# Optimization experiments

Measured on AMD Instinct MI355X. Metric: run time of the kernel, lower is better.

The kernel has to match this reference:

```python
import jax, jax.numpy as jnp
import numpy as np

S, HID, H, KV, D = 2048, 3584, 16, 8, 256
WINDOW = 1024
SOFTCAP = 50.0
SCALING = 256 ** (-0.5)  # query_pre_attn_scalar ** -0.5
EPS = 1e-6
ROPE_THETA = 10000.0


def _rope_tables(seq_len, dim, theta):
    inv_freq = 1.0 / (theta ** (np.arange(0, dim, 2, dtype=np.float32) / dim))
    t = np.arange(seq_len, dtype=np.float32)
    freqs = np.outer(t, inv_freq)            # [S, D/2]
    emb = np.concatenate([freqs, freqs], -1)  # [S, D]
    return jnp.asarray(np.cos(emb)), jnp.asarray(np.sin(emb))


def setup_inputs() -> dict:
    key = jax.random.key(0)
    ks = jax.random.split(key, 3)
    hidden_states = jax.random.normal(ks[0], (S, HID), jnp.float32)
    w_qkv = jax.random.normal(ks[1], (HID, (H + 2 * KV) * D), jnp.float32) * (HID ** -0.5)
    w_o = jax.random.normal(ks[2], (H * D, HID), jnp.float32) * ((H * D) ** -0.5)
    q_norm_w = jnp.zeros((D,), jnp.float32)  # gemma norm stores weight as (1 + w)
    k_norm_w = jnp.zeros((D,), jnp.float32)
    cos, sin = _rope_tables(S, D, ROPE_THETA)
    return {"hidden_states": hidden_states, "w_qkv": w_qkv, "w_o": w_o,
            "q_norm_w": q_norm_w, "k_norm_w": k_norm_w, "cos": cos, "sin": sin}


def _rms_norm(x, w):
    # gemma-style: fp32 norm, scale by (1 + w); x: [S, h, D]
    xf = x.astype(jnp.float32)
    var = jnp.mean(xf * xf, axis=-1, keepdims=True)
    return (xf * jax.lax.rsqrt(var + EPS) * (1.0 + w)).astype(x.dtype)


def _rotate_half(x):
    x1, x2 = jnp.split(x, 2, axis=-1)
    return jnp.concatenate([-x2, x1], axis=-1)


def _apply_rope(x, cos, sin):
    # x: [S, h, D]; cos/sin: [S, D]
    c = cos[:, None, :]
    s = sin[:, None, :]
    return x * c + _rotate_half(x) * s


def reference(hidden_states, w_qkv, w_o, q_norm_w, k_norm_w, cos, sin):
    qkv = hidden_states @ w_qkv                      # [S, (H+2KV)*D]
    q = qkv[:, : H * D].reshape(S, H, D)
    k = qkv[:, H * D: (H + KV) * D].reshape(S, KV, D)
    v = qkv[:, (H + KV) * D:].reshape(S, KV, D)

    q = _rms_norm(q, q_norm_w)                       # gemma3 q_norm
    k = _rms_norm(k, k_norm_w)                       # gemma3 k_norm
    q = _apply_rope(q, cos, sin)
    k = _apply_rope(k, cos, sin)

    # GQA: expand KV heads to H
    rep = H // KV
    k = jnp.repeat(k, rep, axis=1)                   # [S, H, D]
    v = jnp.repeat(v, rep, axis=1)

    scores = jnp.einsum('shd,thd->hst', q, k) * SCALING  # [H, S, S]
    scores = SOFTCAP * jnp.tanh(scores / SOFTCAP)        # logit softcapping

    i = jnp.arange(S)[:, None]
    j = jnp.arange(S)[None, :]
    allowed = (j <= i) & ((i - j) < WINDOW)              # causal + sliding window
    scores = jnp.where(allowed[None], scores, jnp.float32(-1e30))

    attn = jax.nn.softmax(scores, axis=-1)
    out = jnp.einsum('hst,thd->shd', attn, v).reshape(S, H * D)
    return out @ w_o                                     # [S, HID]
```

## Files before the change

### kernel.cpp

```cpp
#include <hip/hip_runtime.h>
#include <hip/hip_bf16.h>
#include <math.h>

typedef __attribute__((ext_vector_type(8))) short short8;
typedef __attribute__((ext_vector_type(4))) float floatx4;
typedef unsigned short u16;

typedef __attribute__((address_space(1))) const void* gas_ptr;
typedef __attribute__((address_space(3))) void* las_ptr;

__device__ __forceinline__ float bf2f(u16 h) {
  union { unsigned u; float f; } v; v.u = ((unsigned)h) << 16; return v.f;
}
__device__ __forceinline__ u16 f2bf(float f) {
  union { float f; unsigned u; } v; v.f = f;
  unsigned r = v.u + 0x7FFFu + ((v.u >> 16) & 1u);
  return (u16)(r >> 16);
}
__device__ __forceinline__ float ldf_dyn(const void* p, size_t i, bool f32) {
  return f32 ? ((const float*)p)[i] : bf2f(((const u16*)p)[i]);
}
__device__ __forceinline__ short8 load8_dyn(const void* p, size_t idx, bool f32) {
  if (f32) {
    const float* f = (const float*)p;
    float4 a = *(const float4*)(f + idx);
    float4 b = *(const float4*)(f + idx + 4);
    short8 r;
    r[0] = (short)f2bf(a.x); r[1] = (short)f2bf(a.y);
    r[2] = (short)f2bf(a.z); r[3] = (short)f2bf(a.w);
    r[4] = (short)f2bf(b.x); r[5] = (short)f2bf(b.y);
    r[6] = (short)f2bf(b.z); r[7] = (short)f2bf(b.w);
    return r;
  }
  return *(const short8*)((const u16*)p + idx);
}
__device__ __forceinline__ void gl_lds16(const u16* g, u16* l) {
  __builtin_amdgcn_global_load_lds((gas_ptr)g, (las_ptr)l, 16, 0, 0);
}

__global__ void probe_dtype_kernel(const void* hidden, int* flag) {
  __shared__ int cnt;
  if (threadIdx.x == 0) cnt = 0;
  __syncthreads();
  const u16* h = (const u16*)hidden;
  int local = 0;
  for (int i = threadIdx.x; i < 8192; i += 256) {
    u16 u = h[i];
    int e = (u >> 7) & 0xFF;
    if ((e >= 64 && e <= 160) || (u & 0x7FFF) == 0) local++;
  }
  atomicAdd(&cnt, local);
  __syncthreads();
  if (threadIdx.x == 0) *flag = (cnt < 7700) ? 1 : 0;
}

__global__ __launch_bounds__(256) void convert_dyn_kernel(
    const void* __restrict__ src, u16* __restrict__ dst, size_t n,
    const int* __restrict__ flagp)
{
  if (*flagp == 0) return;
  size_t i = ((size_t)blockIdx.x * 256 + threadIdx.x) * 8;
  if (i < n) *(short8*)(dst + i) = load8_dyn(src, i, true);
}

__global__ __launch_bounds__(256) void transpose_dyn_kernel(
    const void* __restrict__ src, u16* __restrict__ dst, int R, int C,
    const int* __restrict__ flagp)
{
  const bool f32 = (*flagp != 0);
  const int c0 = blockIdx.x * 64, r0 = blockIdx.y * 64;
  __shared__ __attribute__((aligned(16))) u16 T[64][72];
  const int tid = threadIdx.x;
#pragma unroll
  for (int i = 0; i < 2; i++) {
    int t = tid + i * 256;
    int r = t >> 3, cc = (t & 7) << 3;
    *(short8*)(&T[r][cc]) = load8_dyn(src, (size_t)(r0 + r) * C + c0 + cc, f32);
  }
  __syncthreads();
#pragma unroll
  for (int i = 0; i < 2; i++) {
    int t = tid + i * 256;
    int cr = t >> 3, rc = (t & 7) << 3;
    __attribute__((aligned(16))) u16 tmp[8];
#pragma unroll
    for (int j = 0; j < 8; j++) tmp[j] = T[rc + j][cr];
    *(short8*)(dst + (size_t)(c0 + cr) * R + r0 + rc) = *(const short8*)tmp;
  }
}

#define BAR() __builtin_amdgcn_s_barrier()
#define SCB() __builtin_amdgcn_sched_barrier(0)
#define LGKM0() do { asm volatile("s_waitcnt lgkmcnt(0)" ::: "memory"); SCB(); } while (0)
#define LGKMC(n) do { asm volatile("s_waitcnt lgkmcnt(" #n ")" ::: "memory"); SCB(); } while (0)
#define VMW(n) do { asm volatile("s_waitcnt vmcnt(" #n ")" ::: "memory"); SCB(); } while (0)
#define PRIO1() __builtin_amdgcn_s_setprio(1)
#define PRIO0() do { __builtin_amdgcn_s_setprio(0); SCB(); } while (0)

#define STG_AU(s, u, t) \
  gl_lds16(pa + (size_t)((u) * 64) * K + (size_t)(t) * 64, \
           ldsw + (s) * 32768 + (u) * 4096)
#define STG_BU(s, u, t) \
  gl_lds16(pb + (size_t)((u) * 64) * K + (size_t)(t) * 64, \
           ldsw + (s) * 32768 + 16384 + (u) * 4096)

#define RD_FA(s, miH) do { \
  _Pragma("unroll") \
  for (int m2 = 0; m2 < 4; m2++) { \
    const u16* _r = LDS + (s) * 32768 + wm * 8192 + (miH) * 4096 + m2 * 1024 + lane15 * 64; \
    fa[m2][0] = *(const short8*)(_r + colA0); \
    fa[m2][1] = *(const short8*)(_r + colA1); \
  } \
} while (0)
#define RD_FB(s, niH) do { \
  _Pragma("unroll") \
  for (int n2 = 0; n2 < 2; n2++) { \
    const u16* _r = LDS + (s) * 32768 + 16384 + wn * 4096 + (niH) * 2048 + n2 * 1024 + lane15 * 64; \
    fb[niH][n2][0] = *(const short8*)(_r + colA0); \
    fb[niH][n2][1] = *(const short8*)(_r + colA1); \
  } \
} while (0)
#define RD_FA1(s, miH, m2v) do { \
  const u16* _r = LDS + (s) * 32768 + wm * 8192 + (miH) * 4096 + (m2v) * 1024 + lane15 * 64; \
  fa[m2v][0] = *(const short8*)(_r + colA0); \
  fa[m2v][1] = *(const short8*)(_r + colA1); \
} while (0)
#define RD_FB1(s, niH, n2v) do { \
  const u16* _r = LDS + (s) * 32768 + 16384 + wn * 4096 + (niH) * 2048 + (n2v) * 1024 + lane15 * 64; \
  fb[niH][n2v][0] = *(const short8*)(_r + colA0); \
  fb[niH][n2v][1] = *(const short8*)(_r + colA1); \
} while (0)

#define MFMA_M2(m2v, miH, niH) do { \
  _Pragma("unroll") \
  for (int n2 = 0; n2 < 2; n2++) { \
    acc[(miH) * 4 + (m2v)][(niH) * 2 + n2] = __builtin_amdgcn_mfma_f32_16x16x32_bf16( \
        fa[m2v][0], fb[niH][n2][0], acc[(miH) * 4 + (m2v)][(niH) * 2 + n2], 0, 0, 0); \
    acc[(miH) * 4 + (m2v)][(niH) * 2 + n2] = __builtin_amdgcn_mfma_f32_16x16x32_bf16( \
        fa[m2v][1], fb[niH][n2][1], acc[(miH) * 4 + (m2v)][(niH) * 2 + n2], 0, 0, 0); \
  } \
} while (0)
#define MFMA_N2(n2v, miH, niH) do { \
  _Pragma("unroll") \
  for (int m2 = 0; m2 < 4; m2++) { \
    acc[(miH) * 4 + m2][(niH) * 2 + (n2v)] = __builtin_amdgcn_mfma_f32_16x16x32_bf16( \
        fa[m2][0], fb[niH][n2v][0], acc[(miH) * 4 + m2][(niH) * 2 + (n2v)], 0, 0, 0); \
    acc[(miH) * 4 + m2][(niH) * 2 + (n2v)] = __builtin_amdgcn_mfma_f32_16x16x32_bf16( \
        fa[m2][1], fb[niH][n2v][1], acc[(miH) * 4 + m2][(niH) * 2 + (n2v)], 0, 0, 0); \
  } \
} while (0)
#define MFMA_Q(miH, niH) do { \
  PRIO1(); \
  _Pragma("unroll") \
  for (int m2 = 0; m2 < 4; m2++) \
    _Pragma("unroll") \
    for (int n2 = 0; n2 < 2; n2++) { \
      acc[(miH) * 4 + m2][(niH) * 2 + n2] = __builtin_amdgcn_mfma_f32_16x16x32_bf16( \
          fa[m2][0], fb[niH][n2][0], acc[(miH) * 4 + m2][(niH) * 2 + n2], 0, 0, 0); \
      acc[(miH) * 4 + m2][(niH) * 2 + n2] = __builtin_amdgcn_mfma_f32_16x16x32_bf16( \
          fa[m2][1], fb[niH][n2][1], acc[(miH) * 4 + m2][(niH) * 2 + n2], 0, 0, 0); \
    } \
  PRIO0(); \
} while (0)

__global__ __launch_bounds__(512, 2) void gemm8p_kernel(
    const void* __restrict__ Araw, const u16* __restrict__ Ahb,
    const u16* __restrict__ BT, u16* __restrict__ C,
    int M, int N, int K, const int* __restrict__ flagp)
{
  __shared__ __attribute__((aligned(16))) u16 LDS[65536];
  const int tid = threadIdx.x;
  const int wave = tid >> 6, lane = tid & 63;
  const int lane15 = lane & 15, quad = lane >> 4;
  const int wm = wave >> 2, wn = wave & 3;
  const int m0 = blockIdx.y * 256, n0 = blockIdx.x * 256;

  const u16* Abase = (*flagp != 0) ? Ahb : (const u16*)Araw;

  const int rloc = wave * 8 + (lane >> 3);
  const int sxor = lane >> 3;
  const int csw = ((lane & 7) ^ sxor) * 8;
  const u16* pa = Abase + (size_t)(m0 + rloc) * K + csw;
  const u16* pb = BT + (size_t)(n0 + rloc) * K + csw;
  u16* ldsw = LDS + wave * 512;

  const int swz = lane15 & 7;
  const int colA0 = (quad ^ swz) * 8;
  const int colA1 = ((4 + quad) ^ swz) * 8;

  floatx4 acc[8][4];
#pragma unroll
  for (int i = 0; i < 8; i++)
#pragma unroll
    for (int j = 0; j < 4; j++) acc[i][j] = (floatx4){0.f, 0.f, 0.f, 0.f};
  short8 fa[4][2], fb[2][2][2];

  const int NT = K >> 6, NI = NT >> 1;

  STG_AU(0, 0, 0); STG_AU(0, 2, 0);
  STG_BU(0, 0, 0); STG_BU(0, 1, 0);
  STG_BU(0, 2, 0); STG_BU(0, 3, 0);
  STG_AU(0, 1, 0); STG_AU(0, 3, 0);
  STG_AU(1, 0, 1); STG_AU(1, 2, 1);
  STG_BU(1, 0, 1); STG_BU(1, 1, 1);
  STG_BU(1, 2, 1); STG_BU(1, 3, 1);
  VMW(8);
  BAR();

  for (int i = 0; i < NI - 1; i++) {
    const int t1 = 2 * i + 1, t2 = 2 * i + 2, t3 = 2 * i + 3;
    RD_FB(0, 0); SCB();
    RD_FA1(0, 0, 0); SCB(); RD_FA1(0, 0, 1); SCB();
    RD_FA1(0, 0, 2); SCB(); RD_FA1(0, 0, 3); SCB();
    STG_AU(1, 1, t1); STG_AU(1, 3, t1);
    BAR(); PRIO1();
    LGKMC(6); MFMA_M2(0, 0, 0);
    LGKMC(4); MFMA_M2(1, 0, 0);
    LGKMC(2); MFMA_M2(2, 0, 0);
    LGKM0();  MFMA_M2(3, 0, 0);
    PRIO0(); BAR();
    RD_FB1(0, 1, 0); SCB(); RD_FB1(0, 1, 1); SCB();
    STG_AU(0, 0, t2); STG_AU(0, 2, t2);
    BAR(); PRIO1();
    LGKMC(2); MFMA_N2(0, 0, 1);
    LGKM0();  MFMA_N2(1, 0, 1);
    PRIO0(); VMW(10); BAR();
    RD_FA1(0, 1, 0); SCB(); RD_FA1(0, 1, 1); SCB();
    RD_FA1(0, 1, 2); SCB(); RD_FA1(0, 1, 3); SCB();
    STG_BU(0, 0, t2); STG_BU(0, 1, t2);
    BAR(); PRIO1();
    LGKMC(6); MFMA_M2(0, 1, 1);
    LGKMC(4); MFMA_M2(1, 1, 1);
    LGKMC(2); MFMA_M2(2, 1, 1);
    LGKM0();  MFMA_M2(3, 1, 1);
    PRIO0(); BAR();
    STG_BU(0, 2, t2); STG_BU(0, 3, t2);
    BAR(); MFMA_Q(1, 0); VMW(8); BAR();
    RD_FB(1, 0); SCB();
    RD_FA1(1, 0, 0); SCB(); RD_FA1(1, 0, 1); SCB();
    RD_FA1(1, 0, 2); SCB(); RD_FA1(1, 0, 3); SCB();
    STG_AU(0, 1, t2); STG_AU(0, 3, t2);
    BAR(); PRIO1();
    LGKMC(6); MFMA_M2(0, 0, 0);
    LGKMC(4); MFMA_M2(1, 0, 0);
    LGKMC(2); MFMA_M2(2, 0, 0);
    LGKM0();  MFMA_M2(3, 0, 0);
    PRIO0(); BAR();
    RD_FB1(1, 1, 0); SCB(); RD_FB1(1, 1, 1); SCB();
    STG_AU(1, 0, t3); STG_AU(1, 2, t3);
    BAR(); PRIO1();
    LGKMC(2); MFMA_N2(0, 0, 1);
    LGKM0();  MFMA_N2(1, 0, 1);
    PRIO0(); VMW(10); BAR();
    RD_FA1(1, 1, 0); SCB(); RD_FA1(1, 1, 1); SCB();
    RD_FA1(1, 1, 2); SCB(); RD_FA1(1, 1, 3); SCB();
    STG_BU(1, 0, t3); STG_BU(1, 1, t3);
    BAR(); PRIO1();
    LGKMC(6); MFMA_M2(0, 1, 1);
    LGKMC(4); MFMA_M2(1, 1, 1);
    LGKMC(2); MFMA_M2(2, 1, 1);
    LGKM0();  MFMA_M2(3, 1, 1);
    PRIO0(); BAR();
    STG_BU(1, 2, t3); STG_BU(1, 3, t3);
    BAR(); MFMA_Q(1, 0); VMW(8); BAR();
  }

  {
    const int tL = NT - 1;
    RD_FA(0, 0); RD_FB(0, 0);
    STG_AU(1, 1, tL); STG_AU(1, 3, tL);
    BAR(); LGKM0(); MFMA_Q(0, 0); BAR();
    RD_FB(0, 1);
    BAR(); LGKM0(); MFMA_Q(0, 1); VMW(8); BAR();
    RD_FA(0, 1);
    BAR(); LGKM0(); MFMA_Q(1, 1); BAR();
    BAR(); MFMA_Q(1, 0); VMW(2); BAR();
    RD_FA(1, 0); RD_FB(1, 0);
    BAR(); LGKM0(); MFMA_Q(0, 0); BAR();
    RD_FB(1, 1);
    BAR(); LGKM0(); MFMA_Q(0, 1); VMW(0); BAR();
    RD_FA(1, 1);
    BAR(); LGKM0(); MFMA_Q(1, 1); BAR();
    BAR(); MFMA_Q(1, 0);
  }

#pragma unroll
  for (int mi = 0; mi < 8; mi++)
#pragma unroll
    for (int rr = 0; rr < 4; rr++) {
      int m = m0 + wm * 128 + mi * 16 + quad * 4 + rr;
      u16* crow = C + (size_t)m * N + n0 + wn * 64;
#pragma unroll
      for (int ni = 0; ni < 4; ni++) crow[ni * 16 + lane15] = f2bf(acc[mi][ni][rr]);
    }
}

#define NSTG_A(s, u, t) \
  gl_lds16(pa + (size_t)((u) * 64) * K + (size_t)(t) * 64, \
           ldsw + (s) * 24576 + (u) * 4096)
#define NSTG_B(s, u, t) \
  gl_lds16(pb + (size_t)((u) * 64) * K + (size_t)(t) * 64, \
           ldsw + (s) * 24576 + 8192 + (u) * 4096)

#define NRD_FA(s, miH) do { \
  _Pragma("unroll") \
  for (int m2 = 0; m2 < 2; m2++) { \
    const u16* _r = LDS + (s) * 24576 + wm * 4096 + (miH) * 2048 + m2 * 1024 + lane15 * 64; \
    fa[m2][0] = *(const short8*)(_r + colA0); \
    fa[m2][1] = *(const short8*)(_r + colA1); \
  } \
} while (0)
#define NRD_FB(s, niH) do { \
  _Pragma("unroll") \
  for (int n2 = 0; n2 < 2; n2++) { \
    const u16* _r = LDS + (s) * 24576 + 8192 + wn * 4096 + (niH) * 2048 + n2 * 1024 + lane15 * 64; \
    fb[niH][n2][0] = *(const short8*)(_r + colA0); \
    fb[niH][n2][1] = *(const short8*)(_r + colA1); \
  } \
} while (0)
#define NMFMA_Q(miH, niH) do { \
  PRIO1(); \
  _Pragma("unroll") \
  for (int m2 = 0; m2 < 2; m2++) \
    _Pragma("unroll") \
    for (int n2 = 0; n2 < 2; n2++) { \
      acc[(miH) * 2 + m2][(niH) * 2 + n2] = __builtin_amdgcn_mfma_f32_16x16x32_bf16( \
          fa[m2][0], fb[niH][n2][0], acc[(miH) * 2 + m2][(niH) * 2 + n2], 0, 0, 0); \
      acc[(miH) * 2 + m2][(niH) * 2 + n2] = __builtin_amdgcn_mfma_f32_16x16x32_bf16( \
          fa[m2][1], fb[niH][n2][1], acc[(miH) * 2 + m2][(niH) * 2 + n2], 0, 0, 0); \
    } \
  PRIO0(); \
} while (0)

__global__ __launch_bounds__(512, 2) void gemm8pn_kernel(
    const u16* __restrict__ A, const u16* __restrict__ BT, void* __restrict__ C,
    int M, int N, int K, const int* __restrict__ flagp, int cdyn)
{
  __shared__ __attribute__((aligned(16))) u16 LDS[49152];
  const int tid = threadIdx.x;
  const int wave = tid >> 6, lane = tid & 63;
  const int lane15 = lane & 15, quad = lane >> 4;
  const int wm = wave >> 2, wn = wave & 3;
  const int m0 = blockIdx.y * 128, n0 = blockIdx.x * 256;

  const int rloc = wave * 8 + (lane >> 3);
  const int sxor = lane >> 3;
  const int csw = ((lane & 7) ^ sxor) * 8;
  const u16* pa = A + (size_t)(m0 + rloc) * K + csw;
  const u16* pb = BT + (size_t)(n0 + rloc) * K + csw;
  u16* ldsw = LDS + wave * 512;

  const int swz = lane15 & 7;
  const int colA0 = (quad ^ swz) * 8;
  const int colA1 = ((4 + quad) ^ swz) * 8;

  floatx4 acc[4][4];
#pragma unroll
  for (int i = 0; i < 4; i++)
#pragma unroll
    for (int j = 0; j < 4; j++) acc[i][j] = (floatx4){0.f, 0.f, 0.f, 0.f};
  short8 fa[2][2], fb[2][2][2];

  const int NT = K >> 6, NI = NT >> 1;

  NSTG_B(0, 0, 0); NSTG_B(0, 1, 0); NSTG_B(0, 2, 0); NSTG_B(0, 3, 0);
  NSTG_A(0, 0, 0); NSTG_A(0, 1, 0);
  NSTG_B(1, 0, 1); NSTG_B(1, 1, 1); NSTG_B(1, 2, 1); NSTG_B(1, 3, 1);
  NSTG_A(1, 0, 1); NSTG_A(1, 1, 1);
  VMW(6);
  BAR();

  for (int i = 0; i < NI - 1; i++) {
    const int t2 = 2 * i + 2, t3 = 2 * i + 3;
    NRD_FA(0, 0); NRD_FB(0, 0);
    BAR(); LGKM0(); NMFMA_Q(0, 0); BAR();
    NRD_FB(0, 1);
    BAR(); LGKM0(); NMFMA_Q(0, 1); BAR();
    NRD_FA(0, 1);
    NSTG_B(0, 0, t2); NSTG_B(0, 1, t2);
    BAR(); LGKM0(); NMFMA_Q(1, 1); BAR();
    NSTG_B(0, 2, t2); NSTG_B(0, 3, t2); NSTG_A(0, 0, t2); NSTG_A(0, 1, t2);
    BAR(); NMFMA_Q(1, 0); VMW(6); BAR();
    NRD_FA(1, 0); NRD_FB(1, 0);
    BAR(); LGKM0(); NMFMA_Q(0, 0); BAR();
    NRD_FB(1, 1);
    BAR(); LGKM0(); NMFMA_Q(0, 1); BAR();
    NRD_FA(1, 1);
    NSTG_B(1, 0, t3); NSTG_B(1, 1, t3);
    BAR(); LGKM0(); NMFMA_Q(1, 1); BAR();
    NSTG_B(1, 2, t3); NSTG_B(1, 3, t3); NSTG_A(1, 0, t3); NSTG_A(1, 1, t3);
    BAR(); NMFMA_Q(1, 0); VMW(6); BAR();
  }

  {
    NRD_FA(0, 0); NRD_FB(0, 0);
    BAR(); LGKM0(); NMFMA_Q(0, 0); BAR();
    NRD_FB(0, 1);
    BAR(); LGKM0(); NMFMA_Q(0, 1); BAR();
    NRD_FA(0, 1);
    BAR(); LGKM0(); NMFMA_Q(1, 1); BAR();
    BAR(); NMFMA_Q(1, 0); VMW(0); BAR();
    NRD_FA(1, 0); NRD_FB(1, 0);
    BAR(); LGKM0(); NMFMA_Q(0, 0); BAR();
    NRD_FB(1, 1);
    BAR(); LGKM0(); NMFMA_Q(0, 1); BAR();
    NRD_FA(1, 1);
    BAR(); LGKM0(); NMFMA_Q(1, 1); BAR();
    NMFMA_Q(1, 0);
  }

  const bool cf32 = cdyn && (*flagp != 0);
  if (cf32) {
    float* Cf = (float*)C;
#pragma unroll
    for (int mi = 0; mi < 4; mi++)
#pragma unroll
      for (int rr = 0; rr < 4; rr++) {
        int m = m0 + wm * 64 + mi * 16 + quad * 4 + rr;
        float* crow = Cf + (size_t)m * N + n0 + wn * 64;
#pragma unroll
        for (int ni = 0; ni < 4; ni++) crow[ni * 16 + lane15] = acc[mi][ni][rr];
      }
  } else {
    u16* Cb = (u16*)C;
#pragma unroll
    for (int mi = 0; mi < 4; mi++)
#pragma unroll
      for (int rr = 0; rr < 4; rr++) {
        int m = m0 + wm * 64 + mi * 16 + quad * 4 + rr;
        u16* crow = Cb + (size_t)m * N + n0 + wn * 64;
#pragma unroll
        for (int ni = 0; ni < 4; ni++) crow[ni * 16 + lane15] = f2bf(acc[mi][ni][rr]);
      }
  }
}

__global__ __launch_bounds__(256) void normrope_kernel(
    u16* __restrict__ qkv, const void* __restrict__ qw,
    const void* __restrict__ kw, const void* __restrict__ cosb,
    const void* __restrict__ sinb, const int* __restrict__ flagp)
{
  const bool f32 = (*flagp != 0);
  const int s = blockIdx.x;
  const int wave = threadIdx.x >> 6, lane = threadIdx.x & 63;
  const int hh = blockIdx.y * 4 + wave;
  const int col = (hh < 16) ? hh * 256 : 4096 + (hh - 16) * 256;
  const void* w = (hh < 16) ? qw : kw;
  u16* row = qkv + (size_t)s * 8192 + col;
  const int d0 = lane * 4;

  ushort4 xv = *(const ushort4*)(row + d0);
  float x[4] = {bf2f(xv.x), bf2f(xv.y), bf2f(xv.z), bf2f(xv.w)};

  float ss = x[0] * x[0] + x[1] * x[1] + x[2] * x[2] + x[3] * x[3];
#pragma unroll
  for (int off = 32; off > 0; off >>= 1) ss += __shfl_xor(ss, off);
  float inv = rsqrtf(ss * (1.0f / 256.0f) + 1e-6f);

  float wv[4];
  if (f32) {
    float4 t = *(const float4*)((const float*)w + d0);
    wv[0] = t.x; wv[1] = t.y; wv[2] = t.z; wv[3] = t.w;
  } else {
    ushort4 t = *(const ushort4*)((const u16*)w + d0);
    wv[0] = bf2f(t.x); wv[1] = bf2f(t.y); wv[2] = bf2f(t.z); wv[3] = bf2f(t.w);
  }

  float y[4];
#pragma unroll
  for (int j = 0; j < 4; j++) y[j] = x[j] * inv * (1.0f + wv[j]);

  const float sign = (lane < 32) ? -1.0f : 1.0f;
  float rot[4];
#pragma unroll
  for (int j = 0; j < 4; j++) rot[j] = sign * __shfl_xor(y[j], 32);

  float cv[4], sv[4];
  if (f32) {
    float4 tc = *(const float4*)((const float*)cosb + (size_t)s * 256 + d0);
    float4 ts = *(const float4*)((const float*)sinb + (size_t)s * 256 + d0);
    cv[0] = tc.x; cv[1] = tc.y; cv[2] = tc.z; cv[3] = tc.w;
    sv[0] = ts.x; sv[1] = ts.y; sv[2] = ts.z; sv[3] = ts.w;
  } else {
    ushort4 tc = *(const ushort4*)((const u16*)cosb + (size_t)s * 256 + d0);
    ushort4 ts = *(const ushort4*)((const u16*)sinb + (size_t)s * 256 + d0);
    cv[0] = bf2f(tc.x); cv[1] = bf2f(tc.y); cv[2] = bf2f(tc.z); cv[3] = bf2f(tc.w);
    sv[0] = bf2f(ts.x); sv[1] = bf2f(ts.y); sv[2] = bf2f(ts.z); sv[3] = bf2f(ts.w);
  }

  ushort4 out;
  out.x = f2bf(y[0] * cv[0] + rot[0] * sv[0]);
  out.y = f2bf(y[1] * cv[1] + rot[1] * sv[1]);
  out.z = f2bf(y[2] * cv[2] + rot[2] * sv[2]);
  out.w = f2bf(y[3] * cv[3] + rot[3] * sv[3]);
  *(ushort4*)(row + d0) = out;
}

__global__ __launch_bounds__(256) void vtrans_kernel(
    const u16* __restrict__ qkv, u16* __restrict__ vT)
{
  const int s0 = blockIdx.x * 64, d0 = blockIdx.y * 64, kv = blockIdx.z;
  __shared__ __attribute__((aligned(16))) u16 T[64][72];
  const int tid = threadIdx.x;
#pragma unroll
  for (int i = 0; i < 2; i++) {
    int c = tid + i * 256;
    int r = c >> 3, dc = (c & 7) << 3;
    *(short8*)(&T[r][dc]) =
        *(const short8*)(qkv + (size_t)(s0 + r) * 8192 + 6144 + kv * 256 + d0 + dc);
  }
  __syncthreads();
#pragma unroll
  for (int i = 0; i < 2; i++) {
    int c = tid + i * 256;
    int dr = c >> 3, sc = (c & 7) << 3;
    __attribute__((aligned(16))) u16 tmp[8];
#pragma unroll
    for (int j = 0; j < 8; j++) tmp[j] = T[sc + j][dr];
    *(short8*)(vT + (size_t)kv * 524288 + (size_t)(d0 + dr) * 2048 + s0 + sc) =
        *(const short8*)tmp;
  }
}

__global__ __launch_bounds__(512) void attn_kernel(
    const u16* __restrict__ qkv, const u16* __restrict__ vT,
    u16* __restrict__ aout)
{
  const int h = blockIdx.y, kvh = h >> 1;
  const int q0 = blockIdx.x * 128;
  const int tid = threadIdx.x;
  const int wave = tid >> 6, lane = tid & 63;
  const int lane15 = lane & 15, quad = lane >> 4;

  __shared__ __attribute__((aligned(16))) u16 Ks[64 * 264];
  __shared__ __attribute__((aligned(16))) u16 Vs[256 * 72];
  __shared__ __attribute__((aligned(16))) u16 Ps[8][16 * 72];

  short8 aq[8];
  const u16* qrow = qkv + (size_t)(q0 + wave * 16 + lane15) * 8192 + h * 256;
#pragma unroll
  for (int kt = 0; kt < 8; kt++)
    aq[kt] = *(const short8*)(qrow + kt * 32 + quad * 8);

  floatx4 zero = {0.0f, 0.0f, 0.0f, 0.0f};
  floatx4 accO[16];
#pragma unroll
  for (int i = 0; i < 16; i++) accO[i] = zero;
  float lR[4] = {0.0f, 0.0f, 0.0f, 0.0f};

  const int iRow = q0 + wave * 16 + quad * 4;
  const int kb_lo = (q0 >= 1023) ? ((q0 - 1023) >> 6) : 0;
  const int kb_hi = (q0 + 127) >> 6;

  for (int kb = kb_lo; kb <= kb_hi; kb++) {
    const int t0 = kb << 6;
#pragma unroll
    for (int i = 0; i < 4; i++) {
      int c = tid + i * 512;
      int r = c >> 5, dc = (c & 31) << 3;
      *(short8*)(&Ks[r * 264 + dc]) =
          *(const short8*)(qkv + (size_t)(t0 + r) * 8192 + 4096 + kvh * 256 + dc);
    }
#pragma unroll
    for (int i = 0; i < 4; i++) {
      int c = tid + i * 512;
      int dr = c >> 3, tc = (c & 7) << 3;
      *(short8*)(&Vs[dr * 72 + tc]) =
          *(const short8*)(vT + (size_t)kvh * 524288 + (size_t)dr * 2048 + t0 + tc);
    }
    __syncthreads();

    const int relHi = q0 + 16 * wave + 15 - t0;
    const int relLo = q0 + 16 * wave - 1023 - t0;
    const int niHiR = relHi >> 4;
    const int niHi = (niHiR > 3) ? 3 : niHiR;
    int niLo = relLo >> 4; if (niLo < 0) niLo = 0;
    const int ktHiR = relHi >> 5;
    const int ktHi = (ktHiR > 1) ? 1 : ktHiR;
    int ktLo = relLo >> 5; if (ktLo < 0) ktLo = 0;

    float pv[4][4];
#pragma unroll
    for (int ni = 0; ni < 4; ni++) {
      if (ni < niLo || ni > niHi) {
        pv[ni][0] = pv[ni][1] = pv[ni][2] = pv[ni][3] = 0.0f;
        continue;
      }
      floatx4 sAcc = zero;
#pragma unroll
      for (int kt = 0; kt < 8; kt++) {
        short8 bk = *(const short8*)(&Ks[(ni * 16 + lane15) * 264 + kt * 32 + quad * 8]);
        sAcc = __builtin_amdgcn_mfma_f32_16x16x32_bf16(aq[kt], bk, sAcc, 0, 0, 0);
      }
#pragma unroll
      for (int r = 0; r < 4; r++) {
        float x = sAcc[r] * 0.00125f;
        float ax = __builtin_fabsf(x);
        float e2 = __expf(ax + ax);
        float t = 1.0f - 2.0f * __builtin_amdgcn_rcpf(e2 + 1.0f);
        float sv = copysignf(t, x) * 50.0f;
        int i_ = iRow + r;
        int j_ = t0 + ni * 16 + lane15;
        bool ok = (j_ <= i_) && (i_ - j_ < 1024);
        pv[ni][r] = ok ? __expf(sv) : 0.0f;
      }
    }
#pragma unroll
    for (int r = 0; r < 4; r++)
      lR[r] += pv[0][r] + pv[1][r] + pv[2][r] + pv[3][r];

#pragma unroll
    for (int ni = 0; ni < 4; ni++)
#pragma unroll
      for (int r = 0; r < 4; r++)
        Ps[wave][(quad * 4 + r) * 72 + ni * 16 + lane15] = f2bf(pv[ni][r]);
    __syncthreads();

#pragma unroll
    for (int ktile = 0; ktile < 2; ktile++) {
      if (ktile < ktLo || ktile > ktHi) continue;
      short8 ap = *(const short8*)(&Ps[wave][lane15 * 72 + ktile * 32 + quad * 8]);
#pragma unroll
      for (int ni = 0; ni < 16; ni++) {
        short8 bv = *(const short8*)(&Vs[(ni * 16 + lane15) * 72 + ktile * 32 + quad * 8]);
        accO[ni] = __builtin_amdgcn_mfma_f32_16x16x32_bf16(ap, bv, accO[ni], 0, 0, 0);
      }
    }
    __syncthreads();
  }

#pragma unroll
  for (int r = 0; r < 4; r++) {
    float l = lR[r];
    l += __shfl_xor(l, 1);
    l += __shfl_xor(l, 2);
    l += __shfl_xor(l, 4);
    l += __shfl_xor(l, 8);
    float invl = 1.0f / l;
    u16* orow = aout + (size_t)(q0 + wave * 16 + quad * 4 + r) * 4096 + h * 256;
#pragma unroll
    for (int ni = 0; ni < 16; ni++)
      orow[ni * 16 + lane15] = f2bf(accO[ni][r] * invl);
  }
}

extern "C" void kernel_launch(void* const* d_in, const int* in_sizes, int n_in,
                              void* d_out, int out_size, void* d_ws, size_t ws_size,
                              hipStream_t stream)
{
  const void* hidden = d_in[0];
  const void* w_qkv  = d_in[1];
  const void* w_o    = d_in[2];
  const void* q_w    = d_in[3];
  const void* k_w    = d_in[4];
  const void* cosb   = d_in[5];
  const void* sinb   = d_in[6];

  char* ws = (char*)d_ws;
  int* flag = (int*)ws;                                   ws += 256;
  u16* qkv  = (u16*)ws;  ws += (size_t)2048 * 8192 * 2;
  u16* vT   = (u16*)ws;  ws += (size_t)8 * 256 * 2048 * 2;
  u16* aout = (u16*)ws;  ws += (size_t)2048 * 4096 * 2;
  u16* hb   = (u16*)ws;  ws += (size_t)2048 * 3584 * 2;
  u16* wT   = (u16*)ws;

  probe_dtype_kernel<<<1, 256, 0, stream>>>(hidden, flag);
  convert_dyn_kernel<<<3584, 256, 0, stream>>>(hidden, hb, (size_t)2048 * 3584, flag);
  transpose_dyn_kernel<<<dim3(128, 56), 256, 0, stream>>>(w_qkv, wT, 3584, 8192, flag);
  gemm8p_kernel<<<dim3(32, 8), 512, 0, stream>>>(hidden, hb, wT, qkv, 2048, 8192, 3584, flag);
  normrope_kernel<<<dim3(2048, 6), 256, 0, stream>>>(qkv, q_w, k_w, cosb, sinb, flag);
  transpose_dyn_kernel<<<dim3(56, 64), 256, 0, stream>>>(w_o, wT, 4096, 3584, flag);
  vtrans_kernel<<<dim3(32, 4, 8), 256, 0, stream>>>(qkv, vT);
  attn_kernel<<<dim3(16, 16), 512, 0, stream>>>(qkv, vT, aout);
  gemm8pn_kernel<<<dim3(14, 16), 512, 0, stream>>>(aout, wT, d_out, 2048, 3584, 4096, flag, 1);
}
```

Measured before the change: 518.3 us.

## Switch GEMM mainloop to three-stage LDS ring with fewer barriers

Restructures the gemm8pn mainloop from a two-stage double buffer unrolled by two into a rotating three-stage LDS ring. Each iteration issues global-to-LDS prefetch for tile t+2 right after reading fragments, loads all A fragments at once, and cuts barriers per tile. This aims to hide global load latency and reduce synchronization overhead. It raises LDS use to 144KB per block, which likely prevents two blocks per CU despite the launch bounds, so occupancy may drop.

```diff
diff --git a/kernel.cpp b/kernel.cpp
--- a/kernel.cpp
+++ b/kernel.cpp
@@ -302,41 +302,39 @@
   gl_lds16(pb + (size_t)((u) * 64) * K + (size_t)(t) * 64, \
            ldsw + (s) * 24576 + 8192 + (u) * 4096)
 
-#define NRD_FA(s, miH) do { \
+#define NRD_FA2(s, miH) do { \
   _Pragma("unroll") \
   for (int m2 = 0; m2 < 2; m2++) { \
     const u16* _r = LDS + (s) * 24576 + wm * 4096 + (miH) * 2048 + m2 * 1024 + lane15 * 64; \
-    fa[m2][0] = *(const short8*)(_r + colA0); \
-    fa[m2][1] = *(const short8*)(_r + colA1); \
+    fa2[miH][m2][0] = *(const short8*)(_r + colA0); \
+    fa2[miH][m2][1] = *(const short8*)(_r + colA1); \
   } \
 } while (0)
-#define NRD_FB(s, niH) do { \
+#define NRD_FBC(s, niH) do { \
   _Pragma("unroll") \
   for (int n2 = 0; n2 < 2; n2++) { \
     const u16* _r = LDS + (s) * 24576 + 8192 + wn * 4096 + (niH) * 2048 + n2 * 1024 + lane15 * 64; \
-    fb[niH][n2][0] = *(const short8*)(_r + colA0); \
-    fb[niH][n2][1] = *(const short8*)(_r + colA1); \
+    fbc[n2][0] = *(const short8*)(_r + colA0); \
+    fbc[n2][1] = *(const short8*)(_r + colA1); \
   } \
 } while (0)
-#define NMFMA_Q(miH, niH) do { \
-  PRIO1(); \
+#define NMFMA2(miH, niH) do { \
   _Pragma("unroll") \
   for (int m2 = 0; m2 < 2; m2++) \
     _Pragma("unroll") \
     for (int n2 = 0; n2 < 2; n2++) { \
       acc[(miH) * 2 + m2][(niH) * 2 + n2] = __builtin_amdgcn_mfma_f32_16x16x32_bf16( \
-          fa[m2][0], fb[niH][n2][0], acc[(miH) * 2 + m2][(niH) * 2 + n2], 0, 0, 0); \
+          fa2[miH][m2][0], fbc[n2][0], acc[(miH) * 2 + m2][(niH) * 2 + n2], 0, 0, 0); \
       acc[(miH) * 2 + m2][(niH) * 2 + n2] = __builtin_amdgcn_mfma_f32_16x16x32_bf16( \
-          fa[m2][1], fb[niH][n2][1], acc[(miH) * 2 + m2][(niH) * 2 + n2], 0, 0, 0); \
+          fa2[miH][m2][1], fbc[n2][1], acc[(miH) * 2 + m2][(niH) * 2 + n2], 0, 0, 0); \
     } \
-  PRIO0(); \
 } while (0)
 
 __global__ __launch_bounds__(512, 2) void gemm8pn_kernel(
     const u16* __restrict__ A, const u16* __restrict__ BT, void* __restrict__ C,
     int M, int N, int K, const int* __restrict__ flagp, int cdyn)
 {
-  __shared__ __attribute__((aligned(16))) u16 LDS[49152];
+  __shared__ __attribute__((aligned(16))) u16 LDS[73728];
   const int tid = threadIdx.x;
   const int wave = tid >> 6, lane = tid & 63;
   const int lane15 = lane & 15, quad = lane >> 4;
@@ -359,9 +357,9 @@
   for (int i = 0; i < 4; i++)
 #pragma unroll
     for (int j = 0; j < 4; j++) acc[i][j] = (floatx4){0.f, 0.f, 0.f, 0.f};
-  short8 fa[2][2], fb[2][2][2];
-
-  const int NT = K >> 6, NI = NT >> 1;
+  short8 fa2[2][2][2], fbc[2][2];
+
+  const int NT = K >> 6;
 
   NSTG_B(0, 0, 0); NSTG_B(0, 1, 0); NSTG_B(0, 2, 0); NSTG_B(0, 3, 0);
   NSTG_A(0, 0, 0); NSTG_A(0, 1, 0);
@@ -370,43 +368,33 @@
   VMW(6);
   BAR();
 
-  for (int i = 0; i < NI - 1; i++) {
-    const int t2 = 2 * i + 2, t3 = 2 * i + 3;
-    NRD_FA(0, 0); NRD_FB(0, 0);
-    BAR(); LGKM0(); NMFMA_Q(0, 0); BAR();
-    NRD_FB(0, 1);
-    BAR(); LGKM0(); NMFMA_Q(0, 1); BAR();
-    NRD_FA(0, 1);
-    NSTG_B(0, 0, t2); NSTG_B(0, 1, t2);
-    BAR(); LGKM0(); NMFMA_Q(1, 1); BAR();
-    NSTG_B(0, 2, t2); NSTG_B(0, 3, t2); NSTG_A(0, 0, t2); NSTG_A(0, 1, t2);
-    BAR(); NMFMA_Q(1, 0); VMW(6); BAR();
-    NRD_FA(1, 0); NRD_FB(1, 0);
-    BAR(); LGKM0(); NMFMA_Q(0, 0); BAR();
-    NRD_FB(1, 1);
-    BAR(); LGKM0(); NMFMA_Q(0, 1); BAR();
-    NRD_FA(1, 1);
-    NSTG_B(1, 0, t3); NSTG_B(1, 1, t3);
-    BAR(); LGKM0(); NMFMA_Q(1, 1); BAR();
-    NSTG_B(1, 2, t3); NSTG_B(1, 3, t3); NSTG_A(1, 0, t3); NSTG_A(1, 1, t3);
-    BAR(); NMFMA_Q(1, 0); VMW(6); BAR();
-  }
-
+  int s = 0;
+  for (int t = 0; t < NT - 2; t++) {
+    const int p = (s == 0) ? 2 : s - 1;
+    NRD_FA2(s, 0); NRD_FA2(s, 1); NRD_FBC(s, 0);
+    SCB();
+    NSTG_B(p, 0, t + 2); NSTG_B(p, 1, t + 2);
+    NSTG_B(p, 2, t + 2); NSTG_B(p, 3, t + 2);
+    NSTG_A(p, 0, t + 2); NSTG_A(p, 1, t + 2);
+    BAR(); LGKM0(); PRIO1(); NMFMA2(0, 0); NMFMA2(1, 0); PRIO0(); BAR();
+    NRD_FBC(s, 1);
+    BAR(); LGKM0(); PRIO1(); NMFMA2(0, 1); NMFMA2(1, 1); PRIO0();
+    VMW(6); BAR();
+    s = (s == 2) ? 0 : s + 1;
+  }
   {
-    NRD_FA(0, 0); NRD_FB(0, 0);
-    BAR(); LGKM0(); NMFMA_Q(0, 0); BAR();
-    NRD_FB(0, 1);
-    BAR(); LGKM0(); NMFMA_Q(0, 1); BAR();
-    NRD_FA(0, 1);
-    BAR(); LGKM0(); NMFMA_Q(1, 1); BAR();
-    BAR(); NMFMA_Q(1, 0); VMW(0); BAR();
-    NRD_FA(1, 0); NRD_FB(1, 0);
-    BAR(); LGKM0(); NMFMA_Q(0, 0); BAR();
-    NRD_FB(1, 1);
-    BAR(); LGKM0(); NMFMA_Q(0, 1); BAR();
-    NRD_FA(1, 1);
-    BAR(); LGKM0(); NMFMA_Q(1, 1); BAR();
-    NMFMA_Q(1, 0);
+    NRD_FA2(s, 0); NRD_FA2(s, 1); NRD_FBC(s, 0);
+    BAR(); LGKM0(); PRIO1(); NMFMA2(0, 0); NMFMA2(1, 0); PRIO0(); BAR();
+    NRD_FBC(s, 1);
+    BAR(); LGKM0(); PRIO1(); NMFMA2(0, 1); NMFMA2(1, 1); PRIO0();
+    VMW(0); BAR();
+    s = (s == 2) ? 0 : s + 1;
+  }
+  {
+    NRD_FA2(s, 0); NRD_FA2(s, 1); NRD_FBC(s, 0);
+    BAR(); LGKM0(); PRIO1(); NMFMA2(0, 0); NMFMA2(1, 0); PRIO0(); BAR();
+    NRD_FBC(s, 1);
+    BAR(); LGKM0(); PRIO1(); NMFMA2(0, 1); NMFMA2(1, 1); PRIO0();
   }
 
   const bool cf32 = cdyn && (*flagp != 0);
```

New measurement: 521.7 us. No clear change (+0.7%).
